# Performance work log

Hardware: AMD Instinct MI355X
Metric: run time of the kernel (lower is better)

## Reference

```python
import jax, jax.numpy as jnp
import numpy as np

N = 30000      # nodes
E = 240000     # edges (before self-loops)
D = 128        # vec_dim
L = 6          # GAT layers
NEG_SLOPE = 0.2
EPS = 1e-5


def setup_inputs() -> dict:
    key = jax.random.key(0)
    ks = jax.random.split(key, 20)
    s = 1.0 / np.sqrt(D)
    inp = {
        "x": jax.random.randint(ks[0], (N,), 0, 120),
        "edge_index": jax.random.randint(ks[1], (2, E), 0, N),
        "emb": jax.random.normal(ks[2], (120, D), jnp.float32) * 0.05,
        # stacked GATv2Conv params for 6 layers (heads=1)
        "Wl": jax.random.normal(ks[3], (L, D, D), jnp.float32) * s,
        "bl": jnp.zeros((L, D), jnp.float32),
        "Wr": jax.random.normal(ks[4], (L, D, D), jnp.float32) * s,
        "br": jnp.zeros((L, D), jnp.float32),
        "att": jax.random.normal(ks[5], (L, D), jnp.float32) * s,
        "conv_bias": jnp.zeros((L, D), jnp.float32),
        # PyG LayerNorm (applied after layers 0..4)
        "ln_g": jnp.ones((L - 1, D), jnp.float32),
        "ln_b": jnp.zeros((L - 1, D), jnp.float32),
        # outer Linear + BatchNorm1d
        "lin_W": jax.random.normal(ks[6], (D, D), jnp.float32) * s,
        "lin_b": jnp.zeros((D,), jnp.float32),
        "bn_g": jnp.ones((D,), jnp.float32),
        "bn_b": jnp.zeros((D,), jnp.float32),
    }
    return inp


def _segment_softmax(score, seg, num_segments):
    # numerically stable softmax over variable-degree neighborhoods
    m = jax.ops.segment_max(score, seg, num_segments=num_segments)
    ex = jnp.exp(score - m[seg])
    denom = jax.ops.segment_sum(ex, seg, num_segments=num_segments)
    return ex / denom[seg]


def _gat_forward(h, src, dst, Wl, bl, Wr, br, att, conv_bias, ln_g, ln_b):
    xg = h
    for i in range(L):
        xl = xg @ Wl[i] + bl[i]          # [N, D] source transform
        xr = xg @ Wr[i] + br[i]          # [N, D] target transform
        # GATv2 attention: a^T LeakyReLU(x_l[j] + x_r[i]) per edge j->i
        e = jax.nn.leaky_relu(xl[src] + xr[dst], NEG_SLOPE)   # [E2, D]
        score = e @ att[i]                                     # [E2]
        alpha = _segment_softmax(score, dst, N)                # [E2]
        msg = alpha[:, None] * xl[src]                         # [E2, D]
        xg = jax.ops.segment_sum(msg, dst, num_segments=N) + conv_bias[i]
        if i < L - 1:
            # PyG LayerNorm(mode='graph'): global mean/std, per-channel affine
            mu = xg.mean()
            var = ((xg - mu) ** 2).mean()
            xg = (xg - mu) / jnp.sqrt(var + EPS) * ln_g[i] + ln_b[i]
            xg = jax.nn.relu(xg)
            # dropout(0.1) is identity in eval mode
    return xg


def reference(x, edge_index, emb, Wl, bl, Wr, br, att, conv_bias,
              ln_g, ln_b, lin_W, lin_b, bn_g, bn_b):
    h = emb[x]                                      # [N, D]
    # PyG GATv2Conv default add_self_loops=True
    loops = jnp.arange(N, dtype=edge_index.dtype)
    src = jnp.concatenate([edge_index[0], loops])   # [E2]
    dst = jnp.concatenate([edge_index[1], loops])   # [E2]
    xg = _gat_forward(h, src, dst, Wl, bl, Wr, br, att, conv_bias, ln_g, ln_b)
    out = (h + xg) @ lin_W + lin_b                  # [N, D]
    # BatchNorm1d (batch-statistics / train-mode math)
    mu = out.mean(axis=0)
    var = out.var(axis=0)
    out = (out - mu) / jnp.sqrt(var + EPS) * bn_g + bn_b
    return out
```

## Files before the change

### kernel.cpp

```cpp
#include <hip/hip_runtime.h>
#include <math.h>

#define N_NODES 30000
#define N_EDGES 240000
#define E2 (N_EDGES + N_NODES)
#define D 128
#define LAYERS 6
#define NEG_SLOPE 0.2f
#define LN_EPS 1e-5f

typedef unsigned short u16;
typedef unsigned int u32;
using bfrag = __attribute__((ext_vector_type(8))) short;
using f32x4 = __attribute__((ext_vector_type(4))) float;

__device__ inline u16 f2bf(float f) {
    u32 u = __float_as_uint(f);
    u32 r = u + 0x7fffu + ((u >> 16) & 1u);
    return (u16)(r >> 16);
}
__device__ inline u32 pack2(float a, float b) { return (u32)f2bf(a) | ((u32)f2bf(b) << 16); }
__device__ inline float bflo(u32 u) { return __uint_as_float(u << 16); }
__device__ inline float bfhi(u32 u) { return __uint_as_float(u & 0xffff0000u); }
__device__ inline u32 bfadd2(u32 a, u32 b) {
    return pack2(bflo(a) + bflo(b), bfhi(a) + bfhi(b));
}

__device__ inline float red16_dpp(float x) {
    x += __int_as_float(__builtin_amdgcn_update_dpp(0, __float_as_int(x), 0xB1, 0xF, 0xF, true));
    x += __int_as_float(__builtin_amdgcn_update_dpp(0, __float_as_int(x), 0x4E, 0xF, 0xF, true));
    x += __int_as_float(__builtin_amdgcn_update_dpp(0, __float_as_int(x), 0x141, 0xF, 0xF, true));
    x += __int_as_float(__builtin_amdgcn_update_dpp(0, __float_as_int(x), 0x140, 0xF, 0xF, true));
    return x;
}

__global__ __launch_bounds__(256) void wt_convert(const float* __restrict__ Wl,
        const float* __restrict__ Wr, const float* __restrict__ linW, u16* __restrict__ wt)
{
    __shared__ u16 tile[128 * 129];
    int b = blockIdx.x;
    const float* src = (b == 12) ? linW
                     : ((b & 1) ? Wr + (size_t)(b >> 1) * 16384 : Wl + (size_t)(b >> 1) * 16384);
    int t = threadIdx.x;
    #pragma unroll 4
    for (int i = 0; i < 64; i++) {
        int idx = t + 256 * i;
        int k = idx >> 7, n = idx & 127;
        tile[n * 129 + k] = f2bf(src[idx]);
    }
    __syncthreads();
    u16* dst = wt + (size_t)b * 16384;
    #pragma unroll 4
    for (int i = 0; i < 64; i++) {
        int idx = t + 256 * i;
        int n = idx >> 7, k = idx & 127;
        dst[idx] = tile[n * 129 + k];
    }
}

__global__ __launch_bounds__(256) void hist_kernel(const int* __restrict__ ei, int* __restrict__ cnt)
{
    int e = blockIdx.x * 256 + threadIdx.x;
    if (e >= E2) return;
    int d = (e < N_EDGES) ? ei[N_EDGES + e] : (e - N_EDGES);
    atomicAdd(&cnt[d], 1);
}

__global__ __launch_bounds__(1024) void scan1_kernel(const int* __restrict__ cnt,
        int* __restrict__ lscan, int* __restrict__ bsum)
{
    __shared__ int wtot[16];
    int t = threadIdx.x, lane = t & 63, w = t >> 6;
    int i = blockIdx.x * 1024 + t;
    int v = (i < N_NODES) ? cnt[i] : 0;
    int s = v;
    #pragma unroll
    for (int off = 1; off < 64; off <<= 1) {
        int u = __shfl_up(s, off);
        if (lane >= off) s += u;
    }
    if (lane == 63) wtot[w] = s;
    __syncthreads();
    if (t < 16) {
        int xv = wtot[t];
        #pragma unroll
        for (int off = 1; off < 16; off <<= 1) {
            int u = __shfl_up(xv, off);
            if (t >= off) xv += u;
        }
        wtot[t] = xv;
    }
    __syncthreads();
    int incl = ((w == 0) ? 0 : wtot[w - 1]) + s;
    if (i < N_NODES) lscan[i] = incl;
    if (t == 0) bsum[blockIdx.x] = wtot[15];
}

__global__ __launch_bounds__(1024) void scan3_kernel(const int* __restrict__ lscan,
        const int* __restrict__ bsum, const int* __restrict__ cnt,
        int* __restrict__ row_off, int* __restrict__ cursor)
{
    __shared__ int sboff;
    if (threadIdx.x < 64) {
        int v = (threadIdx.x < 30) ? bsum[threadIdx.x] : 0;
        int s = v;
        #pragma unroll
        for (int off = 1; off < 64; off <<= 1) {
            int u = __shfl_up(s, off);
            if ((int)threadIdx.x >= off) s += u;
        }
        if (threadIdx.x == blockIdx.x) sboff = s - v;
    }
    __syncthreads();
    int i = blockIdx.x * 1024 + threadIdx.x;
    if (i == 0) row_off[0] = 0;
    if (i < N_NODES) {
        int r = lscan[i] + sboff;
        row_off[i + 1] = r;
        cursor[i] = r - cnt[i];
    }
}

__global__ __launch_bounds__(256) void scatter_kernel(const int* __restrict__ ei,
        int* __restrict__ cursor, int* __restrict__ csr_src)
{
    int e = blockIdx.x * 256 + threadIdx.x;
    if (e >= E2) return;
    int s, d;
    if (e < N_EDGES) { s = ei[e]; d = ei[N_EDGES + e]; }
    else             { s = e - N_EDGES; d = s; }
    int pos = atomicAdd(&cursor[d], 1);
    csr_src[pos] = s;
}

template<bool LN, bool OUTF, bool EMB>
__global__ __launch_bounds__(256) void gemm_mfma(
    const u16* __restrict__ Abf, const u16* __restrict__ A2bf,
    const float* __restrict__ Aln, const float* __restrict__ lnacc,
    const float* __restrict__ lng, const float* __restrict__ lnb,
    const int* __restrict__ xidx, const float* __restrict__ emb, u16* __restrict__ h_out,
    const u16* __restrict__ Wt1, const float* __restrict__ b1,
    float* __restrict__ C1f, u16* __restrict__ C1h,
    const u16* __restrict__ Wt2, const float* __restrict__ b2, u16* __restrict__ C2h,
    float* __restrict__ bnacc, int M)
{
    __shared__ u16 As[32 * 136];
    __shared__ float sLN[2];
    const u16*  Wt   = blockIdx.y ? Wt2 : Wt1;
    const float* bias = blockIdx.y ? b2 : b1;
    u16*        Ch   = blockIdx.y ? C2h : C1h;
    int t = threadIdx.x;
    int m0 = blockIdx.x * 32;
    int lane = t & 63, w = t >> 6;
    int n16 = lane & 15, quad = lane >> 4;
    int c0 = w * 32;

    bfrag bW[2][4];
    #pragma unroll
    for (int c = 0; c < 2; c++)
        #pragma unroll
        for (int ks = 0; ks < 4; ks++)
            bW[c][ks] = *(const bfrag*)(Wt + (size_t)(c0 + c * 16 + n16) * 128 + ks * 32 + quad * 8);

    if (LN) {
        if (w == 0) {
            float2 v = ((const float2*)lnacc)[lane];
            float s = v.x, ss = v.y;
            #pragma unroll
            for (int off = 32; off > 0; off >>= 1) {
                s += __shfl_xor(s, off); ss += __shfl_xor(ss, off);
            }
            if (lane == 0) {
                const float invM = 1.f / ((float)N_NODES * (float)D);
                float mu  = s * invM;
                float var = ss * invM - mu * mu;
                sLN[0] = mu;
                sLN[1] = rsqrtf(var + LN_EPS);
            }
        }
        __syncthreads();
        float mu = sLN[0], inv = sLN[1];
        #pragma unroll
        for (int i = 0; i < 4; i++) {
            int idx = t + 256 * i;
            int row = idx >> 5, c4 = idx & 31;
            int gr = m0 + row;
            float4 v = make_float4(0.f, 0.f, 0.f, 0.f);
            if (gr < M) v = ((const float4*)(Aln + (size_t)gr * D))[c4];
            float4 gv = ((const float4*)lng)[c4];
            float4 bv = ((const float4*)lnb)[c4];
            v.x = (v.x - mu) * inv * gv.x + bv.x; v.x = v.x > 0.f ? v.x : 0.f;
            v.y = (v.y - mu) * inv * gv.y + bv.y; v.y = v.y > 0.f ? v.y : 0.f;
            v.z = (v.z - mu) * inv * gv.z + bv.z; v.z = v.z > 0.f ? v.z : 0.f;
            v.w = (v.w - mu) * inv * gv.w + bv.w; v.w = v.w > 0.f ? v.w : 0.f;
            uint2 pk = make_uint2(pack2(v.x, v.y), pack2(v.z, v.w));
            *(uint2*)&As[row * 136 + c4 * 4] = pk;
        }
    } else if (EMB) {
        #pragma unroll
        for (int i = 0; i < 2; i++) {
            int idx = t + 256 * i;
            int row = idx >> 4, c16 = idx & 15;
            int gr = m0 + row;
            uint4 v = make_uint4(0u, 0u, 0u, 0u);
            if (gr < M) {
                const float* er = emb + (size_t)xidx[gr] * D + c16 * 8;
                float4 e0 = ((const float4*)er)[0];
                float4 e1 = ((const float4*)er)[1];
                v.x = pack2(e0.x, e0.y); v.y = pack2(e0.z, e0.w);
                v.z = pack2(e1.x, e1.y); v.w = pack2(e1.z, e1.w);
                if (blockIdx.y == 0)
                    ((uint4*)(h_out + (size_t)gr * 128))[c16] = v;
            }
            *(uint4*)&As[row * 136 + c16 * 8] = v;
        }
    } else {
        #pragma unroll
        for (int i = 0; i < 2; i++) {
            int idx = t + 256 * i;
            int row = idx >> 4, c16 = idx & 15;
            int gr = m0 + row;
            uint4 v = make_uint4(0u, 0u, 0u, 0u);
            if (gr < M) {
                v = ((const uint4*)(Abf + (size_t)gr * 128))[c16];
                if (A2bf) {
                    uint4 u = ((const uint4*)(A2bf + (size_t)gr * 128))[c16];
                    v.x = bfadd2(v.x, u.x); v.y = bfadd2(v.y, u.y);
                    v.z = bfadd2(v.z, u.z); v.w = bfadd2(v.w, u.w);
                }
            }
            *(uint4*)&As[row * 136 + c16 * 8] = v;
        }
    }
    __syncthreads();

    f32x4 zero = {0.f, 0.f, 0.f, 0.f};
    f32x4 acc[2][2] = {{zero, zero}, {zero, zero}};
    #pragma unroll
    for (int ks = 0; ks < 4; ks++) {
        bfrag a[2];
        #pragma unroll
        for (int r = 0; r < 2; r++)
            a[r] = *(const bfrag*)&As[(r * 16 + n16) * 136 + ks * 32 + quad * 8];
        #pragma unroll
        for (int r = 0; r < 2; r++)
            #pragma unroll
            for (int c = 0; c < 2; c++)
                acc[r][c] = __builtin_amdgcn_mfma_f32_16x16x32_bf16(a[r], bW[c][ks], acc[r][c], 0, 0, 0);
    }

    float bv[2] = { bias[c0 + n16], bias[c0 + 16 + n16] };
    float bns[2] = {0.f, 0.f}, bnss[2] = {0.f, 0.f};
    #pragma unroll
    for (int r = 0; r < 2; r++)
        #pragma unroll
        for (int c = 0; c < 2; c++)
            #pragma unroll
            for (int reg = 0; reg < 4; reg++) {
                int grow = m0 + r * 16 + quad * 4 + reg;
                if (grow < M) {
                    float val = acc[r][c][reg] + bv[c];
                    int col = c0 + c * 16 + n16;
                    if (OUTF) {
                        C1f[(size_t)grow * 128 + col] = val;
                        bns[c] += val; bnss[c] += val * val;
                    } else {
                        Ch[(size_t)grow * 128 + col] = f2bf(val);
                    }
                }
            }
    if (OUTF) {
        #pragma unroll
        for (int c = 0; c < 2; c++) {
            #pragma unroll
            for (int msk = 16; msk <= 32; msk <<= 1) {
                bns[c]  += __shfl_xor(bns[c], msk);
                bnss[c] += __shfl_xor(bnss[c], msk);
            }
        }
        if (quad == 0) {
            float* base = bnacc + (size_t)(blockIdx.x & 15) * 256;
            #pragma unroll
            for (int c = 0; c < 2; c++) {
                int col = c0 + c * 16 + n16;
                atomicAdd(&base[col], bns[c]);
                atomicAdd(&base[128 + col], bnss[c]);
            }
        }
    }
}

__global__ __launch_bounds__(256) void gat_agg(
    const u16* __restrict__ xl, const u16* __restrict__ xr,
    const int* __restrict__ row_off, const int* __restrict__ csr_src,
    const float* __restrict__ att, const float* __restrict__ conv_bias,
    float* __restrict__ xg, u16* __restrict__ xg_bf, float* __restrict__ lnacc)
{
    int wave = threadIdx.x >> 6, lane = threadIdx.x & 63;
    int node = blockIdx.x * 4 + wave;
    int g = lane >> 4, q = lane & 15;

    uint4 rr = *(const uint4*)(xr + (size_t)node * 128 + q * 8);
    float4 r0 = make_float4(bflo(rr.x), bfhi(rr.x), bflo(rr.y), bfhi(rr.y));
    float4 r1 = make_float4(bflo(rr.z), bfhi(rr.z), bflo(rr.w), bfhi(rr.w));
    float4 av0 = ((const float4*)att)[2 * q];
    float4 av1 = ((const float4*)att)[2 * q + 1];

    int s0 = row_off[node], s1 = row_off[node + 1];
    float denom = 0.f;
    float4 a0 = make_float4(0.f, 0.f, 0.f, 0.f), a1 = a0;

    #pragma unroll 4
    for (int s = s0 + g; s < s1; s += 4) {
        int src = csr_src[s];
        uint4 raw = *(const uint4*)(xl + (size_t)src * 128 + q * 8);
        float4 v0 = make_float4(bflo(raw.x), bfhi(raw.x), bflo(raw.y), bfhi(raw.y));
        float4 v1 = make_float4(bflo(raw.z), bfhi(raw.z), bflo(raw.w), bfhi(raw.w));
        float pr = 0.f, tt;
        tt = v0.x + r0.x; tt = tt > 0.f ? tt : NEG_SLOPE * tt; pr += av0.x * tt;
        tt = v0.y + r0.y; tt = tt > 0.f ? tt : NEG_SLOPE * tt; pr += av0.y * tt;
        tt = v0.z + r0.z; tt = tt > 0.f ? tt : NEG_SLOPE * tt; pr += av0.z * tt;
        tt = v0.w + r0.w; tt = tt > 0.f ? tt : NEG_SLOPE * tt; pr += av0.w * tt;
        tt = v1.x + r1.x; tt = tt > 0.f ? tt : NEG_SLOPE * tt; pr += av1.x * tt;
        tt = v1.y + r1.y; tt = tt > 0.f ? tt : NEG_SLOPE * tt; pr += av1.y * tt;
        tt = v1.z + r1.z; tt = tt > 0.f ? tt : NEG_SLOPE * tt; pr += av1.z * tt;
        tt = v1.w + r1.w; tt = tt > 0.f ? tt : NEG_SLOPE * tt; pr += av1.w * tt;
        pr = red16_dpp(pr);
        float wv = __expf(pr);
        denom += wv;
        a0.x += wv * v0.x; a0.y += wv * v0.y; a0.z += wv * v0.z; a0.w += wv * v0.w;
        a1.x += wv * v1.x; a1.y += wv * v1.y; a1.z += wv * v1.z; a1.w += wv * v1.w;
    }

    #pragma unroll
    for (int msk = 16; msk <= 32; msk <<= 1) {
        denom += __shfl_xor(denom, msk);
        a0.x += __shfl_xor(a0.x, msk); a0.y += __shfl_xor(a0.y, msk);
        a0.z += __shfl_xor(a0.z, msk); a0.w += __shfl_xor(a0.w, msk);
        a1.x += __shfl_xor(a1.x, msk); a1.y += __shfl_xor(a1.y, msk);
        a1.z += __shfl_xor(a1.z, msk); a1.w += __shfl_xor(a1.w, msk);
    }

    float4 cb0 = ((const float4*)conv_bias)[2 * q];
    float4 cb1 = ((const float4*)conv_bias)[2 * q + 1];
    float inv = 1.f / denom;
    float4 o0, o1;
    o0.x = a0.x * inv + cb0.x; o0.y = a0.y * inv + cb0.y;
    o0.z = a0.z * inv + cb0.z; o0.w = a0.w * inv + cb0.w;
    o1.x = a1.x * inv + cb1.x; o1.y = a1.y * inv + cb1.y;
    o1.z = a1.z * inv + cb1.z; o1.w = a1.w * inv + cb1.w;

    if (xg_bf) {
        if (g == 0) {
            uint4 pk = make_uint4(pack2(o0.x, o0.y), pack2(o0.z, o0.w),
                                  pack2(o1.x, o1.y), pack2(o1.z, o1.w));
            ((uint4*)(xg_bf + (size_t)node * 128))[q] = pk;
        }
    } else {
        if (g == 0) {
            ((float4*)(xg + (size_t)node * 128))[2 * q]     = o0;
            ((float4*)(xg + (size_t)node * 128))[2 * q + 1] = o1;
        }
        float s  = o0.x + o0.y + o0.z + o0.w + o1.x + o1.y + o1.z + o1.w;
        float ss = o0.x*o0.x + o0.y*o0.y + o0.z*o0.z + o0.w*o0.w
                 + o1.x*o1.x + o1.y*o1.y + o1.z*o1.z + o1.w*o1.w;
        s  = red16_dpp(s);
        ss = red16_dpp(ss);
        __shared__ float sred[8];
        if (lane == 0) { sred[wave] = s; sred[4 + wave] = ss; }
        __syncthreads();
        if (threadIdx.x == 0) {
            int slot = blockIdx.x & 63;
            atomicAdd(&lnacc[2 * slot],     sred[0] + sred[1] + sred[2] + sred[3]);
            atomicAdd(&lnacc[2 * slot + 1], sred[4] + sred[5] + sred[6] + sred[7]);
        }
    }
}

__global__ __launch_bounds__(256) void bn_apply(float* __restrict__ out, const float* __restrict__ acc,
        const float* __restrict__ g, const float* __restrict__ b)
{
    int idx = blockIdx.x * 256 + threadIdx.x;
    if (idx >= N_NODES * 32) return;
    int c4 = idx & 31;
    float4 s1 = make_float4(0.f, 0.f, 0.f, 0.f), s2 = s1;
    #pragma unroll
    for (int slot = 0; slot < 16; slot++) {
        float4 a = ((const float4*)(acc + slot * 256))[c4];
        float4 d = ((const float4*)(acc + slot * 256 + 128))[c4];
        s1.x += a.x; s1.y += a.y; s1.z += a.z; s1.w += a.w;
        s2.x += d.x; s2.y += d.y; s2.z += d.z; s2.w += d.w;
    }
    float4 gv = ((const float4*)g)[c4];
    float4 bv = ((const float4*)b)[c4];
    float4 v = ((float4*)out)[idx];
    const float invN = 1.f / (float)N_NODES;
    float mu, var, inv;
    mu = s1.x * invN; var = s2.x * invN - mu * mu; inv = rsqrtf(var + LN_EPS);
    v.x = (v.x - mu) * inv * gv.x + bv.x;
    mu = s1.y * invN; var = s2.y * invN - mu * mu; inv = rsqrtf(var + LN_EPS);
    v.y = (v.y - mu) * inv * gv.y + bv.y;
    mu = s1.z * invN; var = s2.z * invN - mu * mu; inv = rsqrtf(var + LN_EPS);
    v.z = (v.z - mu) * inv * gv.z + bv.z;
    mu = s1.w * invN; var = s2.w * invN - mu * mu; inv = rsqrtf(var + LN_EPS);
    v.w = (v.w - mu) * inv * gv.w + bv.w;
    ((float4*)out)[idx] = v;
}

extern "C" void kernel_launch(void* const* d_in, const int* in_sizes, int n_in,
                              void* d_out, int out_size, void* d_ws, size_t ws_size,
                              hipStream_t stream)
{
    const int*   x    = (const int*)d_in[0];
    const int*   ei   = (const int*)d_in[1];
    const float* emb  = (const float*)d_in[2];
    const float* Wl   = (const float*)d_in[3];
    const float* bl   = (const float*)d_in[4];
    const float* Wr   = (const float*)d_in[5];
    const float* br   = (const float*)d_in[6];
    const float* att  = (const float*)d_in[7];
    const float* cbias= (const float*)d_in[8];
    const float* lng  = (const float*)d_in[9];
    const float* lnb  = (const float*)d_in[10];
    const float* linW = (const float*)d_in[11];
    const float* linb = (const float*)d_in[12];
    const float* bng  = (const float*)d_in[13];
    const float* bnb  = (const float*)d_in[14];
    float* out = (float*)d_out;

    char* p = (char*)d_ws;
    float* xg    = (float*)p; p += (size_t)N_NODES * D * 4;
    u16*   xl_bf = (u16*)p;   p += (size_t)N_NODES * D * 2;
    u16*   xr_bf = (u16*)p;   p += (size_t)N_NODES * D * 2;
    u16*   xg_bf = (u16*)p;   p += (size_t)N_NODES * D * 2;
    u16*   h_bf  = (u16*)p;   p += (size_t)N_NODES * D * 2;
    u16*   wt    = (u16*)p;   p += (size_t)13 * 16384 * 2;
    int* cnt     = (int*)p; p += ((N_NODES * 4 + 255) / 256) * 256;
    int* lscan   = (int*)p; p += ((N_NODES * 4 + 255) / 256) * 256;
    int* row_off = (int*)p; p += (((N_NODES + 1) * 4 + 255) / 256) * 256;
    int* cursor  = (int*)p; p += ((N_NODES * 4 + 255) / 256) * 256;
    int* csr_src = (int*)p; p += ((E2 * 4 + 255) / 256) * 256;
    int* bsum    = (int*)p; p += 256;
    float* accs  = (float*)p; p += 20480;

    hipMemsetAsync(cnt, 0, N_NODES * 4, stream);
    hipMemsetAsync(accs, 0, (640 + 4096) * 4, stream);

    wt_convert<<<13, 256, 0, stream>>>(Wl, Wr, linW, wt);
    hist_kernel<<<(E2 + 255) / 256, 256, 0, stream>>>(ei, cnt);
    scan1_kernel<<<30, 1024, 0, stream>>>(cnt, lscan, bsum);
    scan3_kernel<<<30, 1024, 0, stream>>>(lscan, bsum, cnt, row_off, cursor);
    scatter_kernel<<<(E2 + 255) / 256, 256, 0, stream>>>(ei, cursor, csr_src);

    const int GX = (N_NODES + 31) / 32;
    for (int i = 0; i < LAYERS; i++) {
        if (i == 0) {
            gemm_mfma<false, false, true><<<dim3(GX, 2), 256, 0, stream>>>(
                nullptr, nullptr, nullptr, nullptr, nullptr, nullptr,
                x, emb, h_bf,
                wt + (size_t)0 * 16384, bl + 0, nullptr, xl_bf,
                wt + (size_t)1 * 16384, br + 0, xr_bf, nullptr, N_NODES);
        } else {
            gemm_mfma<true, false, false><<<dim3(GX, 2), 256, 0, stream>>>(
                nullptr, nullptr, xg, accs + (i - 1) * 128,
                lng + (size_t)(i - 1) * D, lnb + (size_t)(i - 1) * D,
                nullptr, nullptr, nullptr,
                wt + (size_t)(2 * i) * 16384, bl + i * D, nullptr, xl_bf,
                wt + (size_t)(2 * i + 1) * 16384, br + i * D, xr_bf, nullptr, N_NODES);
        }
        gat_agg<<<7500, 256, 0, stream>>>(xl_bf, xr_bf, row_off, csr_src,
            att + i * D, cbias + i * D, xg,
            (i == LAYERS - 1) ? xg_bf : nullptr,
            (i < LAYERS - 1) ? (accs + i * 128) : nullptr);
    }
    gemm_mfma<false, true, false><<<dim3(GX, 1), 256, 0, stream>>>(
        xg_bf, h_bf, nullptr, nullptr, nullptr, nullptr,
        nullptr, nullptr, nullptr,
        wt + (size_t)12 * 16384, linb, out, nullptr,
        nullptr, nullptr, nullptr, accs + 640, N_NODES);
    bn_apply<<<3750, 256, 0, stream>>>(out, accs + 640, bng, bnb);
}
```

Measured before the change: 536.1 us.

## Process one edge per full wave in GAT aggregation with batched gathers

Restructures the gat_agg kernel so that each wave handles a node's edges one at a time, with each lane owning two channels, where before four edges ran in parallel across 16-lane groups. Source indices are loaded in chunks of 12 into lanes and broadcast with readlane. All 12 row gathers are issued before any compute, to raise memory-level parallelism. The cross-group shuffle reduction at the end is removed, but every edge now needs a full 64-lane reduction including readlanes, and each gather is a narrower 4-byte access per lane.

Result: slower. 570.3 us (+6.4%).

```diff
diff --git a/kernel.cpp b/kernel.cpp
--- a/kernel.cpp
+++ b/kernel.cpp
@@ -32,6 +32,14 @@
     x += __int_as_float(__builtin_amdgcn_update_dpp(0, __float_as_int(x), 0x141, 0xF, 0xF, true));
     x += __int_as_float(__builtin_amdgcn_update_dpp(0, __float_as_int(x), 0x140, 0xF, 0xF, true));
     return x;
+}
+__device__ inline float red64_dpp(float x) {
+    x = red16_dpp(x);
+    float a = __int_as_float(__builtin_amdgcn_readlane(__float_as_int(x), 0));
+    float b = __int_as_float(__builtin_amdgcn_readlane(__float_as_int(x), 16));
+    float c = __int_as_float(__builtin_amdgcn_readlane(__float_as_int(x), 32));
+    float d = __int_as_float(__builtin_amdgcn_readlane(__float_as_int(x), 48));
+    return (a + b) + (c + d);
 }
 
 __global__ __launch_bounds__(256) void wt_convert(const float* __restrict__ Wl,
@@ -298,74 +306,50 @@
 {
     int wave = threadIdx.x >> 6, lane = threadIdx.x & 63;
     int node = blockIdx.x * 4 + wave;
-    int g = lane >> 4, q = lane & 15;
-
-    uint4 rr = *(const uint4*)(xr + (size_t)node * 128 + q * 8);
-    float4 r0 = make_float4(bflo(rr.x), bfhi(rr.x), bflo(rr.y), bfhi(rr.y));
-    float4 r1 = make_float4(bflo(rr.z), bfhi(rr.z), bflo(rr.w), bfhi(rr.w));
-    float4 av0 = ((const float4*)att)[2 * q];
-    float4 av1 = ((const float4*)att)[2 * q + 1];
+
+    u32 rr = ((const u32*)(xr + (size_t)node * 128))[lane];
+    float rlo = bflo(rr), rhi = bfhi(rr);
+    float2 av = ((const float2*)att)[lane];
+    float2 cb = ((const float2*)conv_bias)[lane];
 
     int s0 = row_off[node], s1 = row_off[node + 1];
-    float denom = 0.f;
-    float4 a0 = make_float4(0.f, 0.f, 0.f, 0.f), a1 = a0;
-
-    #pragma unroll 4
-    for (int s = s0 + g; s < s1; s += 4) {
-        int src = csr_src[s];
-        uint4 raw = *(const uint4*)(xl + (size_t)src * 128 + q * 8);
-        float4 v0 = make_float4(bflo(raw.x), bfhi(raw.x), bflo(raw.y), bfhi(raw.y));
-        float4 v1 = make_float4(bflo(raw.z), bfhi(raw.z), bflo(raw.w), bfhi(raw.w));
-        float pr = 0.f, tt;
-        tt = v0.x + r0.x; tt = tt > 0.f ? tt : NEG_SLOPE * tt; pr += av0.x * tt;
-        tt = v0.y + r0.y; tt = tt > 0.f ? tt : NEG_SLOPE * tt; pr += av0.y * tt;
-        tt = v0.z + r0.z; tt = tt > 0.f ? tt : NEG_SLOPE * tt; pr += av0.z * tt;
-        tt = v0.w + r0.w; tt = tt > 0.f ? tt : NEG_SLOPE * tt; pr += av0.w * tt;
-        tt = v1.x + r1.x; tt = tt > 0.f ? tt : NEG_SLOPE * tt; pr += av1.x * tt;
-        tt = v1.y + r1.y; tt = tt > 0.f ? tt : NEG_SLOPE * tt; pr += av1.y * tt;
-        tt = v1.z + r1.z; tt = tt > 0.f ? tt : NEG_SLOPE * tt; pr += av1.z * tt;
-        tt = v1.w + r1.w; tt = tt > 0.f ? tt : NEG_SLOPE * tt; pr += av1.w * tt;
-        pr = red16_dpp(pr);
-        float wv = __expf(pr);
-        denom += wv;
-        a0.x += wv * v0.x; a0.y += wv * v0.y; a0.z += wv * v0.z; a0.w += wv * v0.w;
-        a1.x += wv * v1.x; a1.y += wv * v1.y; a1.z += wv * v1.z; a1.w += wv * v1.w;
-    }
-
-    #pragma unroll
-    for (int msk = 16; msk <= 32; msk <<= 1) {
-        denom += __shfl_xor(denom, msk);
-        a0.x += __shfl_xor(a0.x, msk); a0.y += __shfl_xor(a0.y, msk);
-        a0.z += __shfl_xor(a0.z, msk); a0.w += __shfl_xor(a0.w, msk);
-        a1.x += __shfl_xor(a1.x, msk); a1.y += __shfl_xor(a1.y, msk);
-        a1.z += __shfl_xor(a1.z, msk); a1.w += __shfl_xor(a1.w, msk);
-    }
-
-    float4 cb0 = ((const float4*)conv_bias)[2 * q];
-    float4 cb1 = ((const float4*)conv_bias)[2 * q + 1];
+    float denom = 0.f, alo = 0.f, ahi = 0.f;
+
+    for (int cs = s0; cs < s1; cs += 12) {
+        int cnt = s1 - cs; cnt = cnt < 12 ? cnt : 12;
+        int csrv = csr_src[(lane < cnt) ? (cs + lane) : cs];
+        u32 vbuf[12];
+        #pragma unroll
+        for (int j = 0; j < 12; j++) {
+            if (j >= cnt) break;
+            int src = __builtin_amdgcn_readlane(csrv, j);
+            vbuf[j] = ((const u32*)(xl + (size_t)src * 128))[lane];
+        }
+        #pragma unroll
+        for (int j = 0; j < 12; j++) {
+            if (j >= cnt) break;
+            u32 v = vbuf[j];
+            float vlo = bflo(v), vhi = bfhi(v);
+            float tlo = vlo + rlo; tlo = tlo > 0.f ? tlo : NEG_SLOPE * tlo;
+            float thi = vhi + rhi; thi = thi > 0.f ? thi : NEG_SLOPE * thi;
+            float pr = av.x * tlo + av.y * thi;
+            float wv = __expf(red64_dpp(pr));
+            denom += wv;
+            alo += wv * vlo;
+            ahi += wv * vhi;
+        }
+    }
+
     float inv = 1.f / denom;
-    float4 o0, o1;
-    o0.x = a0.x * inv + cb0.x; o0.y = a0.y * inv + cb0.y;
-    o0.z = a0.z * inv + cb0.z; o0.w = a0.w * inv + cb0.w;
-    o1.x = a1.x * inv + cb1.x; o1.y = a1.y * inv + cb1.y;
-    o1.z = a1.z * inv + cb1.z; o1.w = a1.w * inv + cb1.w;
+    float olo = alo * inv + cb.x;
+    float ohi = ahi * inv + cb.y;
 
     if (xg_bf) {
-        if (g == 0) {
-            uint4 pk = make_uint4(pack2(o0.x, o0.y), pack2(o0.z, o0.w),
-                                  pack2(o1.x, o1.y), pack2(o1.z, o1.w));
-            ((uint4*)(xg_bf + (size_t)node * 128))[q] = pk;
-        }
+        ((u32*)(xg_bf + (size_t)node * 128))[lane] = pack2(olo, ohi);
     } else {
-        if (g == 0) {
-            ((float4*)(xg + (size_t)node * 128))[2 * q]     = o0;
-            ((float4*)(xg + (size_t)node * 128))[2 * q + 1] = o1;
-        }
-        float s  = o0.x + o0.y + o0.z + o0.w + o1.x + o1.y + o1.z + o1.w;
-        float ss = o0.x*o0.x + o0.y*o0.y + o0.z*o0.z + o0.w*o0.w
-                 + o1.x*o1.x + o1.y*o1.y + o1.z*o1.z + o1.w*o1.w;
-        s  = red16_dpp(s);
-        ss = red16_dpp(ss);
+        ((float2*)(xg + (size_t)node * 128))[lane] = make_float2(olo, ohi);
+        float s  = red64_dpp(olo + ohi);
+        float ss = red64_dpp(olo * olo + ohi * ohi);
         __shared__ float sred[8];
         if (lane == 0) { sred[wave] = s; sred[4 + wave] = ss; }
         __syncthreads();
```
